# Kernel tuning notes

Hardware: AMD Instinct MI355X
Metric: run time of the kernel (lower is better)

## Reference

```python
import jax, jax.numpy as jnp
import numpy as np

B, S, HID, NH, D = 1, 2048, 4096, 32, 128
ROPE_THETA = 10000.0
EPS = 1e-5


def setup_inputs() -> dict:
    key = jax.random.key(0)
    ks = jax.random.split(key, 10)
    w_scale = 1.0 / np.sqrt(HID)
    return {
        "hidden_states": jax.random.normal(ks[0], (B, S, HID), jnp.float32),
        "position_ids": jnp.broadcast_to(jnp.arange(S, dtype=jnp.int32), (B, S)),
        "Wq": jax.random.normal(ks[1], (HID, HID), jnp.float32) * w_scale,
        "Wk": jax.random.normal(ks[2], (HID, HID), jnp.float32) * w_scale,
        "Wv": jax.random.normal(ks[3], (HID, HID), jnp.float32) * w_scale,
        "Wo": jax.random.normal(ks[4], (HID, HID), jnp.float32) * w_scale,
        "qn_w": 1.0 + 0.02 * jax.random.normal(ks[5], (1, D), jnp.float32),
        "qn_b": 0.02 * jax.random.normal(ks[6], (1, D), jnp.float32),
        "kn_w": 1.0 + 0.02 * jax.random.normal(ks[7], (1, D), jnp.float32),
        "kn_b": 0.02 * jax.random.normal(ks[8], (1, D), jnp.float32),
    }


def _head_layernorm(x, gamma, beta, n_heads):
    # x: [B, S, n_heads, D]; gamma/beta: [mp=1, D] repeat-interleaved to [n_heads, D]
    mu = jnp.mean(x, axis=-1, keepdims=True)
    var = jnp.mean(jnp.square(x - mu), axis=-1, keepdims=True)
    xn = (x - mu) * jax.lax.rsqrt(var + EPS)
    g = jnp.repeat(gamma, n_heads // gamma.shape[0], axis=0)  # [n_heads, D]
    b = jnp.repeat(beta, n_heads // beta.shape[0], axis=0)
    return xn * g + b


def _rope_cos_sin(position_ids, dim, dtype):
    inv_freq = 1.0 / (ROPE_THETA ** (jnp.arange(0, dim, 2, dtype=jnp.float32) / dim))
    freqs = position_ids.astype(jnp.float32)[..., None] * inv_freq  # [B, S, D/2]
    emb = jnp.concatenate([freqs, freqs], axis=-1)  # [B, S, D]
    # unsqueeze_dim=-2 -> broadcast over heads in BSND layout
    return jnp.cos(emb)[:, :, None, :].astype(dtype), jnp.sin(emb)[:, :, None, :].astype(dtype)


def _rotate_half(x):
    h = x.shape[-1] // 2
    return jnp.concatenate([-x[..., h:], x[..., :h]], axis=-1)


def reference(hidden_states, position_ids, Wq, Wk, Wv, Wo, qn_w, qn_b, kn_w, kn_b):
    b, s, hid = hidden_states.shape
    d = qn_w.shape[-1]
    nh = hid // d
    nkv = nh  # num_key_value_heads == num_heads for Chameleon-7B (groups=1)

    q = (hidden_states @ Wq).reshape(b, s, nh, d)
    k = (hidden_states @ Wk).reshape(b, s, nkv, d)
    v = (hidden_states @ Wv).reshape(b, s, nkv, d)

    q = _head_layernorm(q, qn_w, qn_b, nh)
    k = _head_layernorm(k, kn_w, kn_b, nkv)

    cos, sin = _rope_cos_sin(position_ids, d, q.dtype)
    q = q * cos + _rotate_half(q) * sin
    k = k * cos + _rotate_half(k) * sin

    scale = d ** -0.5
    scores = jnp.einsum("bqhd,bkhd->bhqk", q, k) * scale  # [B, H, S, S]
    causal = jnp.tril(jnp.ones((s, s), dtype=bool))
    scores = jnp.where(causal[None, None], scores, jnp.finfo(scores.dtype).min)
    probs = jax.nn.softmax(scores, axis=-1)
    attn = jnp.einsum("bhqk,bkhd->bqhd", probs, v).reshape(b, s, hid)
    return attn @ Wo
```

## Files before the change

kernel.cpp:

```cpp
#include <hip/hip_runtime.h>

#define S_LEN 2048
#define HID 4096
#define NH 32
#define HD 128
#define QKV_N 12288

typedef __attribute__((ext_vector_type(8))) short bf16x8;
typedef __attribute__((ext_vector_type(4))) float f32x4;

__device__ __forceinline__ unsigned short f2bf(float f) {
    unsigned int u = __float_as_uint(f);
    u += 0x7FFF + ((u >> 16) & 1);
    return (unsigned short)(u >> 16);
}
__device__ __forceinline__ float bf2f(unsigned short h) {
    return __uint_as_float(((unsigned int)h) << 16);
}

typedef __attribute__((address_space(1))) const void gconst_void;
typedef __attribute__((address_space(3))) void lds_void;
__device__ __forceinline__ void gl16(const void* g, void* l) {
    __builtin_amdgcn_global_load_lds((gconst_void*)g, (lds_void*)l, 16, 0, 0);
}

#define VMCNT(n) asm volatile("s_waitcnt vmcnt(" #n ")" ::: "memory")
#define BAR()    do { asm volatile("" ::: "memory"); __builtin_amdgcn_s_barrier(); asm volatile("" ::: "memory"); } while (0)

__global__ __launch_bounds__(256)
void cvt_f32_bf16(const float* __restrict__ in, unsigned short* __restrict__ out, int n8)
{
    int i = blockIdx.x * 256 + threadIdx.x;
    if (i >= n8) return;
    const float4* p = (const float4*)in + (size_t)i * 2;
    float4 a = p[0], b = p[1];
    bf16x8 o;
    o[0] = (short)f2bf(a.x); o[1] = (short)f2bf(a.y); o[2] = (short)f2bf(a.z); o[3] = (short)f2bf(a.w);
    o[4] = (short)f2bf(b.x); o[5] = (short)f2bf(b.y); o[6] = (short)f2bf(b.z); o[7] = (short)f2bf(b.w);
    *((bf16x8*)out + i) = o;
}

struct W3 { const float* w0; const float* w1; const float* w2; };

__global__ __launch_bounds__(256)
void cvt_w_t3(W3 ws3, unsigned short* __restrict__ Wt, int N, int K)
{
    __shared__ unsigned short t[64][72];
    const float* W = blockIdx.z == 0 ? ws3.w0 : (blockIdx.z == 1 ? ws3.w1 : ws3.w2);
    unsigned short* Wto = Wt + (size_t)blockIdx.z * N * K;
    const int tid = threadIdx.x;
    const int n0 = blockIdx.x * 64, k0 = blockIdx.y * 64;
    const int c4 = (tid & 15) * 4;
    const int r  = tid >> 4;
    #pragma unroll
    for (int p = 0; p < 4; ++p) {
        float4 v = *(const float4*)&W[(size_t)(k0 + r + p * 16) * N + n0 + c4];
        ushort4 o;
        o.x = f2bf(v.x); o.y = f2bf(v.y); o.z = f2bf(v.z); o.w = f2bf(v.w);
        *(ushort4*)&t[r + p * 16][c4] = o;
    }
    __syncthreads();
    const int n = tid >> 2;
    const int kq = (tid & 3) * 16;
    unsigned short* dst = &Wto[(size_t)(n0 + n) * K + k0 + kq];
    bf16x8 v0, v1;
    #pragma unroll
    for (int j = 0; j < 8; ++j) v0[j] = (short)t[kq + j][n];
    #pragma unroll
    for (int j = 0; j < 8; ++j) v1[j] = (short)t[kq + 8 + j][n];
    *(bf16x8*)dst = v0;
    *(bf16x8*)(dst + 8) = v1;
}

template<bool SPLIT>
__global__ __launch_bounds__(256)
void v_transpose(const unsigned short* __restrict__ P0, const unsigned short* __restrict__ P1,
                 unsigned short* __restrict__ Vtg)
{
    __shared__ unsigned short t[64][72];
    const int tid = threadIdx.x;
    const int s0 = blockIdx.x * 64;
    const int c0 = blockIdx.y * 64;
    #pragma unroll
    for (int i = 0; i < 2; ++i) {
        int idx = i * 256 + tid;
        int r = idx >> 3, c8 = (idx & 7) * 8;
        size_t off = (size_t)(s0 + r) * QKV_N + 2 * HID + c0 + c8;
        bf16x8 a = *(const bf16x8*)&P0[off];
        if (SPLIT) {
            bf16x8 b = *(const bf16x8*)&P1[off];
            #pragma unroll
            for (int j = 0; j < 8; ++j)
                a[j] = (short)f2bf(bf2f((unsigned short)a[j]) + bf2f((unsigned short)b[j]));
        }
        *(bf16x8*)&t[r][c8] = a;
    }
    __syncthreads();
    #pragma unroll
    for (int i = 0; i < 2; ++i) {
        int idx = i * 256 + tid;
        int oc = idx >> 3, os8 = (idx & 7) * 8;
        bf16x8 v;
        #pragma unroll
        for (int j = 0; j < 8; ++j) v[j] = (short)t[os8 + j][oc];
        *(bf16x8*)&Vtg[(size_t)(c0 + oc) * S_LEN + s0 + os8] = v;
    }
}

__device__ __forceinline__ void lda4(bf16x8 af[4][2], const char* base, int rq, int l15, int lg) {
    const int sw = (l15 & 7) << 4;
    #pragma unroll
    for (int i = 0; i < 4; ++i) {
        const char* rb = base + ((rq * 4 + i) * 16 + l15) * 128;
        af[i][0] = *(const bf16x8*)(rb + ((lg * 16) ^ sw));
        af[i][1] = *(const bf16x8*)(rb + ((64 + lg * 16) ^ sw));
    }
}
__device__ __forceinline__ void ldb2(bf16x8 bf[2][2], const char* base, int cq, int l15, int lg) {
    const int sw = (l15 & 7) << 4;
    #pragma unroll
    for (int j = 0; j < 2; ++j) {
        const char* rb = base + ((cq * 2 + j) * 16 + l15) * 128;
        bf[j][0] = *(const bf16x8*)(rb + ((lg * 16) ^ sw));
        bf[j][1] = *(const bf16x8*)(rb + ((64 + lg * 16) ^ sw));
    }
}
__device__ __forceinline__ void mfma16(f32x4 acc[8][4], const bf16x8 af[4][2], const bf16x8 bf[2][2],
                                       int mi0, int nj0) {
    __builtin_amdgcn_s_setprio(1);
    #pragma unroll
    for (int kk = 0; kk < 2; ++kk)
        #pragma unroll
        for (int i = 0; i < 4; ++i)
            #pragma unroll
            for (int j = 0; j < 2; ++j)
                acc[mi0 + i][nj0 + j] =
                    __builtin_amdgcn_mfma_f32_16x16x32_bf16(af[i][kk], bf[j][kk], acc[mi0 + i][nj0 + j], 0, 0, 0);
    __builtin_amdgcn_s_setprio(0);
}
__device__ __forceinline__ void stage2(const unsigned short* g, char* dst, int ldk, int r32, int kn) {
    gl16(g + (size_t)r32 * ldk + kn, dst);
    gl16(g + (size_t)(r32 + 8) * ldk + kn, dst + 1024);
}

__global__ __launch_bounds__(512, 2)
void gemm256(const unsigned short* __restrict__ A,
             const unsigned short* __restrict__ Bt,
             unsigned short* __restrict__ Cp,
             int N, int K, int ldk, size_t zstride)
{
    extern __shared__ char lds[];
    const int tid = threadIdx.x;
    const int l   = tid & 63;
    const int l15 = l & 15, lg = l >> 4;
    const int wid = tid >> 6;
    const int wr  = wid >> 2;
    const int wc  = wid & 3;

    const int nwg = gridDim.x;
    const int bid = blockIdx.x;
    const int ntx = N >> 8;
    const int nty = nwg / ntx;
    const int cpx = ntx >> 3;
    const int xcd = bid & 7;
    const int idx = bid >> 3;
    const int bx = xcd * cpx + idx / nty;
    const int by = idx % nty;
    const int m0 = by * 256, n0 = bx * 256;
    const int koff = blockIdx.z * K;

    char* const Abase = lds + wr * 16384;
    char* const Bbase = lds + 32768 + (wc >> 1) * 16384 + (wc & 1) * 8192;

    const int l8 = l >> 3, l7 = l & 7;
    const int swslot = (l7 ^ l8) << 3;

    const unsigned short* Ag = A  + (size_t)(m0 + wr * 128 + wc * 16 + l8) * ldk + koff + swslot;
    const unsigned short* Bg = Bt + (size_t)(n0 + wc * 64 + wr * 16 + l8) * ldk + koff + swslot;
    char* const Adst = Abase + (wc * 16) * 128 + l * 16;
    char* const Bdst = Bbase + (wr * 16) * 128 + l * 16;

    f32x4 acc[8][4] = {};
    bf16x8 af[4][2], bfA[2][2], bfB[2][2];

    stage2(Ag, Adst, ldk, 0, 0);
    stage2(Bg, Bdst, ldk, 0, 0);
    stage2(Ag, Adst + 64 * 128, ldk, 64, 0);
    stage2(Bg, Bdst + 32 * 128, ldk, 32, 0);
    VMCNT(0);
    BAR();

    const int NT = K >> 6;
    for (int t = 0; t < NT; ++t) {
        const int cb = (t & 1) * 65536, nb = cb ^ 65536;
        const int kn = (t + 1) << 6;
        const bool hn = (t + 1) < NT;

        lda4(af, Abase + cb, 0, l15, lg);
        ldb2(bfA, Bbase + cb, 0, l15, lg);
        if (hn) {
            stage2(Ag, Adst + nb, ldk, 0, kn);
            stage2(Bg, Bdst + nb, ldk, 0, kn);
            stage2(Ag, Adst + nb + 64 * 128, ldk, 64, kn);
            stage2(Bg, Bdst + nb + 32 * 128, ldk, 32, kn);
        }
        mfma16(acc, af, bfA, 0, 0);

        ldb2(bfB, Bbase + cb, 1, l15, lg);
        mfma16(acc, af, bfB, 0, 2);

        lda4(af, Abase + cb, 1, l15, lg);
        mfma16(acc, af, bfB, 4, 2);
        mfma16(acc, af, bfA, 4, 0);

        VMCNT(0);
        BAR();
    }

    unsigned short* C = Cp + (size_t)blockIdx.z * zstride;
    const int crow = m0 + wr * 128 + lg * 4;
    const int ccol = n0 + wc * 64 + l15;
    #pragma unroll
    for (int mi = 0; mi < 8; ++mi)
        #pragma unroll
        for (int nj = 0; nj < 4; ++nj)
            #pragma unroll
            for (int rr = 0; rr < 4; ++rr)
                C[(size_t)(crow + mi * 16 + rr) * N + ccol + nj * 16] = f2bf(acc[mi][nj][rr]);
}

__global__ __launch_bounds__(512, 2)
void gemm_wo(const unsigned short* __restrict__ A,
             const unsigned short* __restrict__ Bt,
             float* __restrict__ out, int N, int K)
{
    extern __shared__ char lds[];
    const int tid = threadIdx.x;
    const int l   = tid & 63;
    const int l15 = l & 15, lg = l >> 4;
    const int wid = tid >> 6;
    const int wr  = wid >> 2;
    const int wc  = wid & 3;

    const int bid = blockIdx.x;
    const int ntx = N >> 8;
    const int nty = 256 / ntx;
    const int cpx = ntx >> 3;
    const int xcd = bid & 7;
    const int idx = bid >> 3;
    const int bx = xcd * cpx + idx / nty;
    const int by = idx % nty;
    const int m0 = by * 128, n0 = bx * 256;

    const int r8 = tid >> 3;
    const int swslot = ((tid & 7) ^ (r8 & 7)) << 3;

    const unsigned short* Ag = A  + (size_t)(m0 + r8) * K + swslot;
    const unsigned short* Bg = Bt + (size_t)(n0 + r8) * K + swslot;

    f32x4 acc[4][4] = {};
    bf16x8 af[4][2], bf[4][2];

    #pragma unroll
    for (int i = 0; i < 2; ++i)
        gl16(Ag + (size_t)i * 64 * K, lds + (i * 512 + tid) * 16);
    #pragma unroll
    for (int i = 0; i < 4; ++i)
        gl16(Bg + (size_t)i * 64 * K, lds + 16384 + (i * 512 + tid) * 16);
    VMCNT(0);
    BAR();

    const int NT = K >> 6;
    for (int t = 0; t < NT; ++t) {
        const int cb = (t & 1) * 49152, nb = cb ^ 49152;
        const int kn = (t + 1) << 6;
        const bool hn = (t + 1) < NT;

        const int sw = (l15 & 7) << 4;
        #pragma unroll
        for (int mi = 0; mi < 4; ++mi) {
            const char* rb = lds + cb + (wr * 64 + mi * 16 + l15) * 128;
            af[mi][0] = *(const bf16x8*)(rb + ((lg * 16) ^ sw));
            af[mi][1] = *(const bf16x8*)(rb + ((64 + lg * 16) ^ sw));
        }
        #pragma unroll
        for (int nj = 0; nj < 4; ++nj) {
            const char* rb = lds + cb + 16384 + (wc * 64 + nj * 16 + l15) * 128;
            bf[nj][0] = *(const bf16x8*)(rb + ((lg * 16) ^ sw));
            bf[nj][1] = *(const bf16x8*)(rb + ((64 + lg * 16) ^ sw));
        }
        if (hn) {
            #pragma unroll
            for (int i = 0; i < 2; ++i)
                gl16(Ag + (size_t)i * 64 * K + kn, lds + nb + (i * 512 + tid) * 16);
            #pragma unroll
            for (int i = 0; i < 4; ++i)
                gl16(Bg + (size_t)i * 64 * K + kn, lds + nb + 16384 + (i * 512 + tid) * 16);
        }
        __builtin_amdgcn_s_setprio(1);
        #pragma unroll
        for (int kk = 0; kk < 2; ++kk)
            #pragma unroll
            for (int mi = 0; mi < 4; ++mi)
                #pragma unroll
                for (int nj = 0; nj < 4; ++nj)
                    acc[mi][nj] = __builtin_amdgcn_mfma_f32_16x16x32_bf16(af[mi][kk], bf[nj][kk], acc[mi][nj], 0, 0, 0);
        __builtin_amdgcn_s_setprio(0);

        VMCNT(0);
        BAR();
    }

    const int crow = m0 + wr * 64 + lg * 4;
    const int ccol = n0 + wc * 64 + l15;
    #pragma unroll
    for (int mi = 0; mi < 4; ++mi)
        #pragma unroll
        for (int nj = 0; nj < 4; ++nj)
            #pragma unroll
            for (int rr = 0; rr < 4; ++rr)
                out[(size_t)(crow + mi * 16 + rr) * N + ccol + nj * 16] = acc[mi][nj][rr];
}

template<bool SPLIT>
__global__ __launch_bounds__(256)
void ln_rope(unsigned short* __restrict__ P0, const unsigned short* __restrict__ P1,
             const float* __restrict__ qg, const float* __restrict__ qb,
             const float* __restrict__ kg, const float* __restrict__ kb,
             const int* __restrict__ pos)
{
    const int tid = threadIdx.x;
    const int l = tid & 63;
    const int w = tid >> 6;
    const int rid = blockIdx.x * 4 + w;
    const int s = rid >> 6;
    const int hh = rid & 63;
    const int which = hh >> 5;
    const int h = hh & 31;
    const size_t off = (size_t)s * QKV_N + which * HID + h * HD;
    unsigned short* p = P0 + off;
    const float* gamma = which ? kg : qg;
    const float* beta  = which ? kb : qb;

    float lo = bf2f(p[l]);
    float hi = bf2f(p[l + 64]);
    if (SPLIT) {
        const unsigned short* q = P1 + off;
        lo += bf2f(q[l]);
        hi += bf2f(q[l + 64]);
    }
    float sum = lo + hi;
    #pragma unroll
    for (int off2 = 32; off2 >= 1; off2 >>= 1) sum += __shfl_xor(sum, off2, 64);
    float mu = sum * (1.0f / 128.0f);
    float dlo = lo - mu, dhi = hi - mu;
    float vs = dlo * dlo + dhi * dhi;
    #pragma unroll
    for (int off2 = 32; off2 >= 1; off2 >>= 1) vs += __shfl_xor(vs, off2, 64);
    float rstd = rsqrtf(vs * (1.0f / 128.0f) + 1e-5f);
    float xlo = dlo * rstd * gamma[l] + beta[l];
    float xhi = dhi * rstd * gamma[l + 64] + beta[l + 64];

    float fpos = (float)pos[s];
    float invf = exp2f(-13.287712379549449f * (float)l * (1.0f / 64.0f));
    float ang = fpos * invf;
    float sn, cs;
    sincosf(ang, &sn, &cs);
    p[l]      = f2bf(xlo * cs - xhi * sn);
    p[l + 64] = f2bf(xhi * cs + xlo * sn);
}

#define KVB 128
#define ATTN_LDS 149504

__global__ __launch_bounds__(512)
void attn_fwd(const unsigned short* __restrict__ QKV,
              const unsigned short* __restrict__ Vtg,
              unsigned short* __restrict__ O)
{
    extern __shared__ char shb[];
    unsigned short* const Psw = (unsigned short*)(shb + 131072) + (threadIdx.x >> 6) * (16 * 72);

    const int tid = threadIdx.x;
    const int l = tid & 63;
    const int w = tid >> 6;
    const int l15 = l & 15, lg = l >> 4;
    const int h = blockIdx.y;
    const int qb = gridDim.x - 1 - blockIdx.x;
    const int q0 = qb * 128;
    const int qw = q0 + w * 16;

    const unsigned short* Qp = QKV + h * HD;
    const unsigned short* Kp = QKV + HID + h * HD;
    const unsigned short* Vp = Vtg + (size_t)h * HD * S_LEN;

    bf16x8 qf[4];
    #pragma unroll
    for (int d = 0; d < 4; ++d)
        qf[d] = *(const bf16x8*)&Qp[(size_t)(qw + l15) * QKV_N + d * 32 + lg * 8];

    f32x4 o_acc[8] = {};
    float mgrp = -1e30f;
    float lsum[4] = {0.0f, 0.0f, 0.0f, 0.0f};

    const float scale = 0.08838834764831845f;

    const int ksl = tid & 15;
    const int kr7 = (tid >> 4) & 7;
    const int ksg = (ksl & 8) | ((ksl ^ kr7) & 7);
    const unsigned short* Kg = Kp + (size_t)(tid >> 4) * QKV_N + ksg * 8;
    const unsigned short* Vg = Vp + (size_t)(tid >> 4) * S_LEN + ksg * 8;

#define STAGE(buf, kv0s) do {                                                          \
    _Pragma("unroll")                                                                  \
    for (int i_ = 0; i_ < 4; ++i_)                                                     \
        gl16(Kg + (size_t)((kv0s) + i_ * 32) * QKV_N,                                  \
             shb + (buf) * 32768 + (i_ * 512 + tid) * 16);                             \
    _Pragma("unroll")                                                                  \
    for (int i_ = 0; i_ < 4; ++i_)                                                     \
        gl16(Vg + (size_t)i_ * 32 * S_LEN + (kv0s),                                    \
             shb + 65536 + (buf) * 32768 + (i_ * 512 + tid) * 16);                     \
} while (0)

    STAGE(0, 0);
    VMCNT(0);
    __syncthreads();

    const int nt = qb + 1;
    for (int t = 0; t < nt; ++t) {
        const int kv0 = t * KVB;
        const int cur = t & 1;
        const bool hn = (t + 1) < nt;
        if (hn) STAGE(cur ^ 1, kv0 + KVB);

        f32x4 sc[8] = {};
        const char* Kb = shb + cur * 32768;
        #pragma unroll
        for (int kvf = 0; kvf < 8; ++kvf) {
            int r = kvf * 16 + l15;
            int sw = (r & 7) << 4;
            #pragma unroll
            for (int d = 0; d < 4; ++d) {
                bf16x8 kf = *(const bf16x8*)(Kb + r * 256 + ((d * 64 + lg * 16) ^ sw));
                sc[kvf] = __builtin_amdgcn_mfma_f32_16x16x32_bf16(qf[d], kf, sc[kvf], 0, 0, 0);
            }
        }

        const bool full = (kv0 + KVB <= qw);
        if (!full) {
            #pragma unroll
            for (int k = 0; k < 8; ++k) {
                #pragma unroll
                for (int r = 0; r < 4; ++r) {
                    int qg = qw + lg * 4 + r;
                    if (kv0 + k * 16 + l15 > qg) sc[k][r] = -1e30f;
                }
            }
        }
        float mx = fmaxf(fmaxf(sc[0][0], sc[0][1]), fmaxf(sc[0][2], sc[0][3]));
        #pragma unroll
        for (int k = 1; k < 8; ++k) {
            float m2 = fmaxf(fmaxf(sc[k][0], sc[k][1]), fmaxf(sc[k][2], sc[k][3]));
            mx = fmaxf(mx, m2);
        }
        mx *= scale;
        #pragma unroll
        for (int off = 8; off >= 1; off >>= 1) mx = fmaxf(mx, __shfl_xor(mx, off, 64));
        if (!__all(mx <= mgrp + 8.0f)) {
            float mn = fmaxf(mgrp, mx);
            float corr = __expf(mgrp - mn);
            #pragma unroll
            for (int r = 0; r < 4; ++r) lsum[r] *= corr;
            #pragma unroll
            for (int df = 0; df < 8; ++df) o_acc[df] *= corr;
            mgrp = mn;
        }
        const float mn = mgrp;

        float ph[4][4];
        #pragma unroll
        for (int r = 0; r < 4; ++r) {
            int ql = lg * 4 + r;
            float psum = 0.0f;
            #pragma unroll
            for (int k = 0; k < 8; ++k) {
                float p = __expf(fmaf(sc[k][r], scale, -mn));
                psum += p;
                if (k < 4) Psw[ql * 72 + k * 16 + l15] = f2bf(p);
                else       ph[r][k - 4] = p;
            }
            lsum[r] += psum;
        }

        const char* Vb = shb + 65536 + cur * 32768;
        {
            bf16x8 pa0 = *(const bf16x8*)&Psw[l15 * 72 + lg * 8];
            bf16x8 pa1 = *(const bf16x8*)&Psw[l15 * 72 + 32 + lg * 8];
            #pragma unroll
            for (int df = 0; df < 8; ++df) {
                int d = df * 16 + l15;
                int sw = (d & 7) << 4;
                const char* vrow = Vb + d * 256;
                bf16x8 v0 = *(const bf16x8*)(vrow + ((lg * 16) ^ sw));
                bf16x8 v1 = *(const bf16x8*)(vrow + ((64 + lg * 16) ^ sw));
                o_acc[df] = __builtin_amdgcn_mfma_f32_16x16x32_bf16(pa0, v0, o_acc[df], 0, 0, 0);
                o_acc[df] = __builtin_amdgcn_mfma_f32_16x16x32_bf16(pa1, v1, o_acc[df], 0, 0, 0);
            }
        }
        #pragma unroll
        for (int r = 0; r < 4; ++r) {
            int ql = lg * 4 + r;
            #pragma unroll
            for (int k = 0; k < 4; ++k)
                Psw[ql * 72 + k * 16 + l15] = f2bf(ph[r][k]);
        }
        {
            bf16x8 pa0 = *(const bf16x8*)&Psw[l15 * 72 + lg * 8];
            bf16x8 pa1 = *(const bf16x8*)&Psw[l15 * 72 + 32 + lg * 8];
            #pragma unroll
            for (int df = 0; df < 8; ++df) {
                int d = df * 16 + l15;
                int sw = (d & 7) << 4;
                const char* vrow = Vb + d * 256;
                bf16x8 v0 = *(const bf16x8*)(vrow + ((128 + lg * 16) ^ sw));
                bf16x8 v1 = *(const bf16x8*)(vrow + ((128 + 64 + lg * 16) ^ sw));
                o_acc[df] = __builtin_amdgcn_mfma_f32_16x16x32_bf16(pa0, v0, o_acc[df], 0, 0, 0);
                o_acc[df] = __builtin_amdgcn_mfma_f32_16x16x32_bf16(pa1, v1, o_acc[df], 0, 0, 0);
            }
        }

        if (hn) {
            VMCNT(0);
            BAR();
        }
    }
#undef STAGE

    float inv[4];
    #pragma unroll
    for (int r = 0; r < 4; ++r) {
        float s = lsum[r];
        #pragma unroll
        for (int off = 8; off >= 1; off >>= 1) s += __shfl_xor(s, off, 64);
        inv[r] = 1.0f / s;
    }
    #pragma unroll
    for (int df = 0; df < 8; ++df) {
        #pragma unroll
        for (int r = 0; r < 4; ++r) {
            int q = qw + lg * 4 + r;
            int d = h * HD + df * 16 + l15;
            O[(size_t)q * HID + d] = f2bf(o_acc[df][r] * inv[r]);
        }
    }
}

extern "C" void kernel_launch(void* const* d_in, const int* in_sizes, int n_in,
                              void* d_out, int out_size, void* d_ws, size_t ws_size,
                              hipStream_t stream)
{
    (void)in_sizes; (void)n_in; (void)out_size;
    const float* X    = (const float*)d_in[0];
    const int*   pos  = (const int*)d_in[1];
    const float* Wq   = (const float*)d_in[2];
    const float* Wk   = (const float*)d_in[3];
    const float* Wv   = (const float*)d_in[4];
    const float* Wo   = (const float*)d_in[5];
    const float* qn_w = (const float*)d_in[6];
    const float* qn_b = (const float*)d_in[7];
    const float* kn_w = (const float*)d_in[8];
    const float* kn_b = (const float*)d_in[9];
    float* out = (float*)d_out;

    unsigned short* Xb    = (unsigned short*)d_ws;
    unsigned short* QKVb  = (unsigned short*)((char*)d_ws + 16777216);
    unsigned short* Wt    = (unsigned short*)((char*)d_ws + 67108864);
    unsigned short* Vtg   = (unsigned short*)((char*)d_ws + 134217728);
    unsigned short* P1    = (unsigned short*)((char*)d_ws + 167772160);
    unsigned short* Ab    = Xb;

    const bool splitQKV = ws_size >= (size_t)218103808;

    (void)hipFuncSetAttribute((const void*)gemm256, hipFuncAttributeMaxDynamicSharedMemorySize, 131072);
    (void)hipFuncSetAttribute((const void*)gemm_wo, hipFuncAttributeMaxDynamicSharedMemorySize, 98304);
    (void)hipFuncSetAttribute((const void*)attn_fwd, hipFuncAttributeMaxDynamicSharedMemorySize, ATTN_LDS);

    dim3 blk(256);

    cvt_f32_bf16<<<dim3((S_LEN * HID / 8 + 255) / 256), blk, 0, stream>>>(X, Xb, S_LEN * HID / 8);

    W3 w3{Wq, Wk, Wv};
    cvt_w_t3<<<dim3(HID / 64, HID / 64, 3), blk, 0, stream>>>(w3, Wt, HID, HID);

    if (splitQKV) {
        gemm256<<<dim3(384, 1, 2), dim3(512), 131072, stream>>>(
            Xb, Wt, QKVb, QKV_N, HID / 2, HID, (size_t)75497472);
        v_transpose<true><<<dim3(S_LEN / 64, HID / 64), blk, 0, stream>>>(QKVb, P1, Vtg);
        ln_rope<true><<<dim3(S_LEN * 64 / 4), blk, 0, stream>>>(QKVb, P1, qn_w, qn_b, kn_w, kn_b, pos);
    } else {
        gemm256<<<dim3(384, 1, 1), dim3(512), 131072, stream>>>(
            Xb, Wt, QKVb, QKV_N, HID, HID, (size_t)0);
        v_transpose<false><<<dim3(S_LEN / 64, HID / 64), blk, 0, stream>>>(QKVb, QKVb, Vtg);
        ln_rope<false><<<dim3(S_LEN * 64 / 4), blk, 0, stream>>>(QKVb, QKVb, qn_w, qn_b, kn_w, kn_b, pos);
    }

    attn_fwd<<<dim3(S_LEN / 128, NH), dim3(512), ATTN_LDS, stream>>>(QKVb, Vtg, Ab);

    W3 wo3{Wo, Wo, Wo};
    cvt_w_t3<<<dim3(HID / 64, HID / 64, 1), blk, 0, stream>>>(wo3, Wt, HID, HID);

    gemm_wo<<<dim3(256), dim3(512), 98304, stream>>>(Ab, Wt, out, HID, HID);
}
```

Before: 475.4 us.

## Rework QKV GEMM to 1024-thread blocks with BK=32 double buffering

Replaces the 512-thread QKV GEMM kernel (BK=64, 8 waves each computing a 128x64 sub-tile, 128 KB LDS) with a 1024-thread variant. In the new kernel 16 waves each compute a 64x64 sub-tile, with a K step of 32, 64 KB of LDS and one global-to-LDS load per thread per operand. The aim is more waves per block to hide latency and less LDS per block. The cost is twice as many loop iterations and barriers, plus a lower MFMA-to-LDS-read ratio per wave.

```diff
diff --git a/kernel.cpp b/kernel.cpp
--- a/kernel.cpp
+++ b/kernel.cpp
@@ -107,47 +107,11 @@
     }
 }
 
-__device__ __forceinline__ void lda4(bf16x8 af[4][2], const char* base, int rq, int l15, int lg) {
-    const int sw = (l15 & 7) << 4;
-    #pragma unroll
-    for (int i = 0; i < 4; ++i) {
-        const char* rb = base + ((rq * 4 + i) * 16 + l15) * 128;
-        af[i][0] = *(const bf16x8*)(rb + ((lg * 16) ^ sw));
-        af[i][1] = *(const bf16x8*)(rb + ((64 + lg * 16) ^ sw));
-    }
-}
-__device__ __forceinline__ void ldb2(bf16x8 bf[2][2], const char* base, int cq, int l15, int lg) {
-    const int sw = (l15 & 7) << 4;
-    #pragma unroll
-    for (int j = 0; j < 2; ++j) {
-        const char* rb = base + ((cq * 2 + j) * 16 + l15) * 128;
-        bf[j][0] = *(const bf16x8*)(rb + ((lg * 16) ^ sw));
-        bf[j][1] = *(const bf16x8*)(rb + ((64 + lg * 16) ^ sw));
-    }
-}
-__device__ __forceinline__ void mfma16(f32x4 acc[8][4], const bf16x8 af[4][2], const bf16x8 bf[2][2],
-                                       int mi0, int nj0) {
-    __builtin_amdgcn_s_setprio(1);
-    #pragma unroll
-    for (int kk = 0; kk < 2; ++kk)
-        #pragma unroll
-        for (int i = 0; i < 4; ++i)
-            #pragma unroll
-            for (int j = 0; j < 2; ++j)
-                acc[mi0 + i][nj0 + j] =
-                    __builtin_amdgcn_mfma_f32_16x16x32_bf16(af[i][kk], bf[j][kk], acc[mi0 + i][nj0 + j], 0, 0, 0);
-    __builtin_amdgcn_s_setprio(0);
-}
-__device__ __forceinline__ void stage2(const unsigned short* g, char* dst, int ldk, int r32, int kn) {
-    gl16(g + (size_t)r32 * ldk + kn, dst);
-    gl16(g + (size_t)(r32 + 8) * ldk + kn, dst + 1024);
-}
-
-__global__ __launch_bounds__(512, 2)
-void gemm256(const unsigned short* __restrict__ A,
-             const unsigned short* __restrict__ Bt,
-             unsigned short* __restrict__ Cp,
-             int N, int K, int ldk, size_t zstride)
+__global__ __launch_bounds__(1024)
+void gemm_qkv(const unsigned short* __restrict__ A,
+              const unsigned short* __restrict__ Bt,
+              unsigned short* __restrict__ Cp,
+              int N, int K, int ldk, size_t zstride)
 {
     extern __shared__ char lds[];
     const int tid = threadIdx.x;
@@ -169,59 +133,58 @@
     const int m0 = by * 256, n0 = bx * 256;
     const int koff = blockIdx.z * K;
 
-    char* const Abase = lds + wr * 16384;
-    char* const Bbase = lds + 32768 + (wc >> 1) * 16384 + (wc & 1) * 8192;
-
-    const int l8 = l >> 3, l7 = l & 7;
-    const int swslot = (l7 ^ l8) << 3;
-
-    const unsigned short* Ag = A  + (size_t)(m0 + wr * 128 + wc * 16 + l8) * ldk + koff + swslot;
-    const unsigned short* Bg = Bt + (size_t)(n0 + wc * 64 + wr * 16 + l8) * ldk + koff + swslot;
-    char* const Adst = Abase + (wc * 16) * 128 + l * 16;
-    char* const Bdst = Bbase + (wr * 16) * 128 + l * 16;
-
-    f32x4 acc[8][4] = {};
-    bf16x8 af[4][2], bfA[2][2], bfB[2][2];
-
-    stage2(Ag, Adst, ldk, 0, 0);
-    stage2(Bg, Bdst, ldk, 0, 0);
-    stage2(Ag, Adst + 64 * 128, ldk, 64, 0);
-    stage2(Bg, Bdst + 32 * 128, ldk, 32, 0);
+    const int sr = tid >> 2;
+    const int sc = tid & 3;
+    const int sg = sc ^ (sr & 3);
+    const unsigned short* Ag = A  + (size_t)(m0 + sr) * ldk + koff + sg * 8;
+    const unsigned short* Bg = Bt + (size_t)(n0 + sr) * ldk + koff + sg * 8;
+    const int dstA = tid * 16;
+    const int dstB = 16384 + tid * 16;
+
+    f32x4 acc[4][4] = {};
+    bf16x8 af[4], bf[4];
+
+    gl16(Ag, lds + dstA);
+    gl16(Bg, lds + dstB);
     VMCNT(0);
     BAR();
 
-    const int NT = K >> 6;
+    const int NT = K >> 5;
     for (int t = 0; t < NT; ++t) {
-        const int cb = (t & 1) * 65536, nb = cb ^ 65536;
-        const int kn = (t + 1) << 6;
+        const int cb = (t & 1) * 32768, nb = cb ^ 32768;
+        const int kn = (t + 1) << 5;
         const bool hn = (t + 1) < NT;
 
-        lda4(af, Abase + cb, 0, l15, lg);
-        ldb2(bfA, Bbase + cb, 0, l15, lg);
+        #pragma unroll
+        for (int mi = 0; mi < 4; ++mi) {
+            int row = wr * 64 + mi * 16 + l15;
+            af[mi] = *(const bf16x8*)(lds + cb + row * 64 + ((lg ^ (row & 3)) << 4));
+        }
+        #pragma unroll
+        for (int nj = 0; nj < 4; ++nj) {
+            int row = wc * 64 + nj * 16 + l15;
+            bf[nj] = *(const bf16x8*)(lds + cb + 16384 + row * 64 + ((lg ^ (row & 3)) << 4));
+        }
         if (hn) {
-            stage2(Ag, Adst + nb, ldk, 0, kn);
-            stage2(Bg, Bdst + nb, ldk, 0, kn);
-            stage2(Ag, Adst + nb + 64 * 128, ldk, 64, kn);
-            stage2(Bg, Bdst + nb + 32 * 128, ldk, 32, kn);
-        }
-        mfma16(acc, af, bfA, 0, 0);
-
-        ldb2(bfB, Bbase + cb, 1, l15, lg);
-        mfma16(acc, af, bfB, 0, 2);
-
-        lda4(af, Abase + cb, 1, l15, lg);
-        mfma16(acc, af, bfB, 4, 2);
-        mfma16(acc, af, bfA, 4, 0);
-
+            gl16(Ag + kn, lds + nb + dstA);
+            gl16(Bg + kn, lds + nb + dstB);
+        }
+        __builtin_amdgcn_s_setprio(1);
+        #pragma unroll
+        for (int mi = 0; mi < 4; ++mi)
+            #pragma unroll
+            for (int nj = 0; nj < 4; ++nj)
+                acc[mi][nj] = __builtin_amdgcn_mfma_f32_16x16x32_bf16(af[mi], bf[nj], acc[mi][nj], 0, 0, 0);
+        __builtin_amdgcn_s_setprio(0);
         VMCNT(0);
         BAR();
     }
 
     unsigned short* C = Cp + (size_t)blockIdx.z * zstride;
-    const int crow = m0 + wr * 128 + lg * 4;
+    const int crow = m0 + wr * 64 + lg * 4;
     const int ccol = n0 + wc * 64 + l15;
     #pragma unroll
-    for (int mi = 0; mi < 8; ++mi)
+    for (int mi = 0; mi < 4; ++mi)
         #pragma unroll
         for (int nj = 0; nj < 4; ++nj)
             #pragma unroll
@@ -581,7 +544,7 @@
 
     const bool splitQKV = ws_size >= (size_t)218103808;
 
-    (void)hipFuncSetAttribute((const void*)gemm256, hipFuncAttributeMaxDynamicSharedMemorySize, 131072);
+    (void)hipFuncSetAttribute((const void*)gemm_qkv, hipFuncAttributeMaxDynamicSharedMemorySize, 65536);
     (void)hipFuncSetAttribute((const void*)gemm_wo, hipFuncAttributeMaxDynamicSharedMemorySize, 98304);
     (void)hipFuncSetAttribute((const void*)attn_fwd, hipFuncAttributeMaxDynamicSharedMemorySize, ATTN_LDS);
 
@@ -593,12 +556,12 @@
     cvt_w_t3<<<dim3(HID / 64, HID / 64, 3), blk, 0, stream>>>(w3, Wt, HID, HID);
 
     if (splitQKV) {
-        gemm256<<<dim3(384, 1, 2), dim3(512), 131072, stream>>>(
+        gemm_qkv<<<dim3(384, 1, 2), dim3(1024), 65536, stream>>>(
             Xb, Wt, QKVb, QKV_N, HID / 2, HID, (size_t)75497472);
         v_transpose<true><<<dim3(S_LEN / 64, HID / 64), blk, 0, stream>>>(QKVb, P1, Vtg);
         ln_rope<true><<<dim3(S_LEN * 64 / 4), blk, 0, stream>>>(QKVb, P1, qn_w, qn_b, kn_w, kn_b, pos);
     } else {
-        gemm256<<<dim3(384, 1, 1), dim3(512), 131072, stream>>>(
+        gemm_qkv<<<dim3(384, 1, 1), dim3(1024), 65536, stream>>>(
             Xb, Wt, QKVb, QKV_N, HID, HID, (size_t)0);
         v_transpose<false><<<dim3(S_LEN / 64, HID / 64), blk, 0, stream>>>(QKVb, QKVb, Vtg);
         ln_rope<false><<<dim3(S_LEN * 64 / 4), blk, 0, stream>>>(QKVb, QKVb, qn_w, qn_b, kn_w, kn_b, pos);
```

Result: slower. 500.2 us (+5.2%).
